# Performance work log

Hardware: AMD Instinct MI355X
Metric: run time of the kernel (lower is better)

Reference implementation:

```python
import jax, jax.numpy as jnp
import numpy as np

WINDOW_SIZE = 11
SIGMA = 1.5
C1 = 0.01 ** 2
C2 = 0.03 ** 2


def _gaussian_window(window_size: int = WINDOW_SIZE, sigma: float = SIGMA) -> jnp.ndarray:
    x = np.arange(window_size)
    g = np.exp(-((x - window_size // 2) ** 2) / (2.0 * sigma ** 2)).astype(np.float32)
    g = g / g.sum()
    w2d = np.outer(g, g)  # [K, K]
    return jnp.asarray(w2d[None, None])  # [1, 1, K, K] (OIHW)


def _blur(x: jnp.ndarray, window: jnp.ndarray) -> jnp.ndarray:
    pad = WINDOW_SIZE // 2
    return jax.lax.conv_general_dilated(
        x, window, window_strides=(1, 1),
        padding=[(pad, pad), (pad, pad)],
        dimension_numbers=("NCHW", "OIHW", "NCHW"))


def setup_inputs() -> dict:
    key = jax.random.key(0)
    k1, k2 = jax.random.split(key)
    shape = (16, 1, 1024, 1024)
    img1 = jax.random.uniform(k1, shape, dtype=jnp.float32)
    img2 = jax.random.uniform(k2, shape, dtype=jnp.float32)
    return {"img1": img1, "img2": img2}


def reference(img1, img2) -> jnp.ndarray:
    window = _gaussian_window().astype(img1.dtype)
    mu1 = _blur(img1, window)
    mu2 = _blur(img2, window)
    mu1_sq = mu1 * mu1
    mu2_sq = mu2 * mu2
    mu1_mu2 = mu1 * mu2
    sigma1_sq = _blur(img1 * img1, window) - mu1_sq
    sigma2_sq = _blur(img2 * img2, window) - mu2_sq
    sigma12 = _blur(img1 * img2, window) - mu1_mu2
    ssim_map = ((2 * mu1_mu2 + C1) * (2 * sigma12 + C2)) / (
        (mu1_sq + mu2_sq + C1) * (sigma1_sq + sigma2_sq + C2))
    return 1.0 - ssim_map.mean()
```

## Files before the change

### kernel.cpp

```cpp
#include <hip/hip_runtime.h>
#include <hip/hip_fp16.h>

#define IMG_H 1024
#define IMG_W 1024
#define NIMG  16
#define RAD   5
#define KW    11
#define TX    64
#define STRIP 128
#define ASTEP 16
#define BSTEP 32
#define HBROWS (STRIP + 2*RAD)
#define RING  48
#define PADW  68
#define NPIX  (NIMG * IMG_H * IMG_W)

__device__ __forceinline__ float gw(int k) {
    constexpr float G[KW] = {
        0.00102838f, 0.00759876f, 0.03600077f, 0.10936070f, 0.21300554f,
        0.26601173f,
        0.21300554f, 0.10936070f, 0.03600077f, 0.00759876f, 0.00102838f};
    return G[k];
}

__device__ __forceinline__ unsigned h2u(__half2 v) {
    union { __half2 h; unsigned u; } c; c.h = v; return c.u;
}
__device__ __forceinline__ __half2 u2h(unsigned v) {
    union { unsigned u; __half2 h; } c; c.u = v; return c.h;
}
__device__ __forceinline__ __half2 hsel(const unsigned* hw, int idx) {
    unsigned r;
    if (idx & 1) r = (hw[idx >> 1] >> 16) | (hw[(idx >> 1) + 1] << 16);
    else         r = hw[idx >> 1];
    return u2h(r);
}

__global__ __launch_bounds__(256, 8) void ssim_strip_kernel(
        const float* __restrict__ img1, const float* __restrict__ img2,
        float* __restrict__ partial, int atomic_mode) {
    __shared__ __align__(16) __half hb[5][RING][PADW];
    __shared__ float wsum[4];

    const int t = threadIdx.x;
    const int tile_x = blockIdx.x * TX;
    const int tile_y = blockIdx.y * STRIP;
    const size_t img_off = (size_t)blockIdx.z * (IMG_H * IMG_W);
    const float* p1 = img1 + img_off;
    const float* p2 = img2 + img_off;

    const bool x_ok = (tile_x >= 8) && (tile_x + 72 <= IMG_W);

    auto phaseA = [&](int a) {
        const int tr = t >> 4;
        const int g4 = t & 15;
        const int h = ASTEP * a + tr;
        if (h >= HBROWS) return;
        int rr = h;
        if (rr >= 96) rr -= 96;
        else if (rr >= RING) rr -= RING;
        const int gr = tile_y + h - RAD;
        const int gc0 = tile_x + g4 * 4 - 8;
        const bool row_ok = (tile_y + ASTEP * a - RAD >= 0) &&
                            (tile_y + ASTEP * a + ASTEP - 1 - RAD < IMG_H);
        unsigned hwx[10], hwy[10];
        if (x_ok && row_ok) {
            const size_t base = (size_t)gr * IMG_W + gc0;
#pragma unroll
            for (int w = 0; w < 5; ++w) {
                const float4 xa = *reinterpret_cast<const float4*>(p1 + base + 4 * w);
                const float4 ya = *reinterpret_cast<const float4*>(p2 + base + 4 * w);
                hwx[2 * w]     = h2u(__floats2half2_rn(xa.x, xa.y));
                hwx[2 * w + 1] = h2u(__floats2half2_rn(xa.z, xa.w));
                hwy[2 * w]     = h2u(__floats2half2_rn(ya.x, ya.y));
                hwy[2 * w + 1] = h2u(__floats2half2_rn(ya.z, ya.w));
            }
        } else {
            const bool rowok = ((unsigned)gr < (unsigned)IMG_H);
            const float* row1 = p1 + (size_t)gr * IMG_W;
            const float* row2 = p2 + (size_t)gr * IMG_W;
#pragma unroll
            for (int w = 0; w < 5; ++w) {
                const int gc = gc0 + 4 * w;
                float4 xa = make_float4(0.f, 0.f, 0.f, 0.f);
                float4 ya = make_float4(0.f, 0.f, 0.f, 0.f);
                if (rowok) {
                    if (gc >= 0 && gc <= IMG_W - 4) {
                        xa = *reinterpret_cast<const float4*>(row1 + gc);
                        ya = *reinterpret_cast<const float4*>(row2 + gc);
                    } else if (gc > -4 && gc < IMG_W) {
                        float* ex = &xa.x;
                        float* ey = &ya.x;
#pragma unroll
                        for (int j = 0; j < 4; ++j) {
                            int g = gc + j;
                            if ((unsigned)g < (unsigned)IMG_W) {
                                ex[j] = row1[g];
                                ey[j] = row2[g];
                            }
                        }
                    }
                }
                hwx[2 * w]     = h2u(__floats2half2_rn(xa.x, xa.y));
                hwx[2 * w + 1] = h2u(__floats2half2_rn(xa.z, xa.w));
                hwy[2 * w]     = h2u(__floats2half2_rn(ya.x, ya.y));
                hwy[2 * w + 1] = h2u(__floats2half2_rn(ya.z, ya.w));
            }
        }
        __half2 A0[2], A1[2], A2[2], A3[2], A4[2];
#pragma unroll
        for (int p = 0; p < 2; ++p)
            A0[p] = A1[p] = A2[p] = A3[p] = A4[p] = u2h(0u);
#pragma unroll
        for (int k = 0; k < KW; ++k) {
            const __half2 g2 = __float2half2_rn(gw(k));
#pragma unroll
            for (int p = 0; p < 2; ++p) {
                const int idx = 2 * p + 3 + k;
                const __half2 X = hsel(hwx, idx);
                const __half2 Y = hsel(hwy, idx);
                A0[p] = __hfma2(g2, X, A0[p]);
                A1[p] = __hfma2(g2, Y, A1[p]);
                const __half2 gx = __hmul2(g2, X);
                const __half2 gy = __hmul2(g2, Y);
                A2[p] = __hfma2(gx, X, A2[p]);
                A3[p] = __hfma2(gy, Y, A3[p]);
                A4[p] = __hfma2(gx, Y, A4[p]);
            }
        }
        *reinterpret_cast<uint2*>(&hb[0][rr][g4 * 4]) = make_uint2(h2u(A0[0]), h2u(A0[1]));
        *reinterpret_cast<uint2*>(&hb[1][rr][g4 * 4]) = make_uint2(h2u(A1[0]), h2u(A1[1]));
        *reinterpret_cast<uint2*>(&hb[2][rr][g4 * 4]) = make_uint2(h2u(A2[0]), h2u(A2[1]));
        *reinterpret_cast<uint2*>(&hb[3][rr][g4 * 4]) = make_uint2(h2u(A3[0]), h2u(A3[1]));
        *reinterpret_cast<uint2*>(&hb[4][rr][g4 * 4]) = make_uint2(h2u(A4[0]), h2u(A4[1]));
    };

    float lsum = 0.f;

    auto phaseB = [&](int s) {
        __half2 gh2[KW];
#pragma unroll
        for (int k = 0; k < KW; ++k) gh2[k] = __float2half2_rn(gw(k));

        const int rbase = (BSTEP * s) % RING;
        const int slot = t & 15;
        const int r2 = (t >> 4) * 2;
        __half2 acc[5][2][2];
#pragma unroll
        for (int q = 0; q < 5; ++q)
#pragma unroll
            for (int rl = 0; rl < 2; ++rl)
#pragma unroll
                for (int cp = 0; cp < 2; ++cp)
                    acc[q][rl][cp] = u2h(0u);

#pragma unroll
        for (int q = 0; q < 5; ++q) {
#pragma unroll
            for (int k = 0; k < KW + 1; ++k) {
                int r = rbase + r2 + k;
                if (r >= RING) r -= RING;
                const uint2 rv =
                    *reinterpret_cast<const uint2*>(&hb[q][r][slot * 4]);
                __half2 h0 = u2h(rv.x);
                __half2 h1 = u2h(rv.y);
                if (k < KW) {
                    acc[q][0][0] = __hfma2(gh2[k], h0, acc[q][0][0]);
                    acc[q][0][1] = __hfma2(gh2[k], h1, acc[q][0][1]);
                }
                if (k > 0) {
                    acc[q][1][0] = __hfma2(gh2[k - 1], h0, acc[q][1][0]);
                    acc[q][1][1] = __hfma2(gh2[k - 1], h1, acc[q][1][1]);
                }
            }
        }

        const float C1 = 0.0001f;
        const float C2 = 0.0009f;
#pragma unroll
        for (int rl = 0; rl < 2; ++rl) {
#pragma unroll
            for (int cp = 0; cp < 2; ++cp) {
                float2 m1p  = __half22float2(acc[0][rl][cp]);
                float2 m2p  = __half22float2(acc[1][rl][cp]);
                float2 b11p = __half22float2(acc[2][rl][cp]);
                float2 b22p = __half22float2(acc[3][rl][cp]);
                float2 b12p = __half22float2(acc[4][rl][cp]);
#pragma unroll
                for (int e = 0; e < 2; ++e) {
                    float m1 = e ? m1p.y : m1p.x;
                    float m2 = e ? m2p.y : m2p.x;
                    float b11 = e ? b11p.y : b11p.x;
                    float b22 = e ? b22p.y : b22p.x;
                    float b12 = e ? b12p.y : b12p.x;
                    float m1s = m1 * m1;
                    float m2s = m2 * m2;
                    float m12 = m1 * m2;
                    float num = (2.f * m12 + C1) * (2.f * (b12 - m12) + C2);
                    float den = (m1s + m2s + C1) *
                                ((b11 - m1s) + (b22 - m2s) + C2);
                    lsum = fmaf(num, __builtin_amdgcn_rcpf(den), lsum);
                }
            }
        }
    };

#pragma unroll 1
    for (int a = 0; a < 9; ++a) {
        phaseA(a);
        __syncthreads();
        if (a >= 2 && ((a & 1) == 0)) {
            phaseB((a - 2) >> 1);
            __syncthreads();
        }
    }

#pragma unroll
    for (int off = 32; off > 0; off >>= 1)
        lsum += __shfl_down(lsum, off, 64);
    if ((t & 63) == 0) wsum[t >> 6] = lsum;
    __syncthreads();
    if (t == 0) {
        float s = wsum[0] + wsum[1] + wsum[2] + wsum[3];
        if (atomic_mode) {
            atomicAdd(partial, s);
        } else {
            int bid = (blockIdx.z * gridDim.y + blockIdx.y) * gridDim.x + blockIdx.x;
            partial[bid] = s;
        }
    }
}

__global__ __launch_bounds__(256) void ssim_reduce_kernel(
        const float* __restrict__ partial, int n, float* __restrict__ out) {
    float s = 0.f;
    for (int i = threadIdx.x; i < n; i += 256) s += partial[i];
#pragma unroll
    for (int off = 32; off > 0; off >>= 1)
        s += __shfl_down(s, off, 64);
    __shared__ float ws[4];
    if ((threadIdx.x & 63) == 0) ws[threadIdx.x >> 6] = s;
    __syncthreads();
    if (threadIdx.x == 0) {
        float tot = ws[0] + ws[1] + ws[2] + ws[3];
        out[0] = 1.f - tot / (float)NPIX;
    }
}

extern "C" void kernel_launch(void* const* d_in, const int* in_sizes, int n_in,
                              void* d_out, int out_size, void* d_ws, size_t ws_size,
                              hipStream_t stream) {
    const float* img1 = (const float*)d_in[0];
    const float* img2 = (const float*)d_in[1];
    float* out = (float*)d_out;
    float* partial = (float*)d_ws;

    dim3 grid(IMG_W / TX, IMG_H / STRIP, NIMG);
    const int nblocks = (IMG_W / TX) * (IMG_H / STRIP) * NIMG;
    const size_t needed = (size_t)nblocks * sizeof(float);

    if (ws_size >= needed) {
        ssim_strip_kernel<<<grid, 256, 0, stream>>>(img1, img2, partial, 0);
        ssim_reduce_kernel<<<1, 256, 0, stream>>>(partial, nblocks, out);
    } else {
        hipMemsetAsync(d_ws, 0, sizeof(float), stream);
        ssim_strip_kernel<<<grid, 256, 0, stream>>>(img1, img2, partial, 1);
        ssim_reduce_kernel<<<1, 256, 0, stream>>>(partial, 1, out);
    }
}
```

Baseline: 79.56 us.

## Prefetch next strip rows into registers while computing the vertical SSIM pass

Splits the horizontal pass into a global-load step and a convert/blur/store step, so raw float4 row data can be loaded into registers before the vertical-blur and SSIM phase runs and consumed after the barrier. The aim is to hide global memory latency behind the phase-B compute instead of stalling at the start of each horizontal step. The loop is unrolled into a software pipeline with fewer barriers. Launch bounds drop from 8 to 4 blocks per CU to leave room for the extra live registers, which risks lower occupancy.

New measurement: 165.5 us. 108% more time.

```diff
diff --git a/kernel.cpp b/kernel.cpp
--- a/kernel.cpp
+++ b/kernel.cpp
@@ -36,7 +36,12 @@
     return u2h(r);
 }
 
-__global__ __launch_bounds__(256, 8) void ssim_strip_kernel(
+struct Raw {
+    float4 x0, x1, x2, x3, x4;
+    float4 y0, y1, y2, y3, y4;
+};
+
+__global__ __launch_bounds__(256, 4) void ssim_strip_kernel(
         const float* __restrict__ img1, const float* __restrict__ img2,
         float* __restrict__ partial, int atomic_mode) {
     __shared__ __align__(16) __half hb[5][RING][PADW];
@@ -51,7 +56,65 @@
 
     const bool x_ok = (tile_x >= 8) && (tile_x + 72 <= IMG_W);
 
-    auto phaseA = [&](int a) {
+    auto ldpair = [&](const float* r1, const float* r2, int gc, bool rowok,
+                      float4& xa, float4& ya) {
+        xa = make_float4(0.f, 0.f, 0.f, 0.f);
+        ya = make_float4(0.f, 0.f, 0.f, 0.f);
+        if (rowok) {
+            if (gc >= 0 && gc <= IMG_W - 4) {
+                xa = *reinterpret_cast<const float4*>(r1 + gc);
+                ya = *reinterpret_cast<const float4*>(r2 + gc);
+            } else if (gc > -4 && gc < IMG_W) {
+                float* ex = &xa.x;
+                float* ey = &ya.x;
+#pragma unroll
+                for (int j = 0; j < 4; ++j) {
+                    int g = gc + j;
+                    if ((unsigned)g < (unsigned)IMG_W) {
+                        ex[j] = r1[g];
+                        ey[j] = r2[g];
+                    }
+                }
+            }
+        }
+    };
+
+    auto loadRaw = [&](int a) -> Raw {
+        Raw rw;
+        const int tr = t >> 4;
+        const int g4 = t & 15;
+        const int h = ASTEP * a + tr;
+        const int gr = tile_y + h - RAD;
+        const int gc0 = tile_x + g4 * 4 - 8;
+        const bool row_ok = (tile_y + ASTEP * a - RAD >= 0) &&
+                            (tile_y + ASTEP * a + ASTEP - 1 - RAD < IMG_H);
+        if (h < HBROWS && x_ok && row_ok) {
+            const float* b1 = p1 + (size_t)gr * IMG_W + gc0;
+            const float* b2 = p2 + (size_t)gr * IMG_W + gc0;
+            rw.x0 = *reinterpret_cast<const float4*>(b1);
+            rw.x1 = *reinterpret_cast<const float4*>(b1 + 4);
+            rw.x2 = *reinterpret_cast<const float4*>(b1 + 8);
+            rw.x3 = *reinterpret_cast<const float4*>(b1 + 12);
+            rw.x4 = *reinterpret_cast<const float4*>(b1 + 16);
+            rw.y0 = *reinterpret_cast<const float4*>(b2);
+            rw.y1 = *reinterpret_cast<const float4*>(b2 + 4);
+            rw.y2 = *reinterpret_cast<const float4*>(b2 + 8);
+            rw.y3 = *reinterpret_cast<const float4*>(b2 + 12);
+            rw.y4 = *reinterpret_cast<const float4*>(b2 + 16);
+        } else {
+            const bool rowok = (h < HBROWS) && ((unsigned)gr < (unsigned)IMG_H);
+            const float* r1 = p1 + (size_t)gr * IMG_W;
+            const float* r2 = p2 + (size_t)gr * IMG_W;
+            ldpair(r1, r2, gc0,      rowok, rw.x0, rw.y0);
+            ldpair(r1, r2, gc0 + 4,  rowok, rw.x1, rw.y1);
+            ldpair(r1, r2, gc0 + 8,  rowok, rw.x2, rw.y2);
+            ldpair(r1, r2, gc0 + 12, rowok, rw.x3, rw.y3);
+            ldpair(r1, r2, gc0 + 16, rowok, rw.x4, rw.y4);
+        }
+        return rw;
+    };
+
+    auto blurStore = [&](const Raw& rw, int a) {
         const int tr = t >> 4;
         const int g4 = t & 15;
         const int h = ASTEP * a + tr;
@@ -59,54 +122,28 @@
         int rr = h;
         if (rr >= 96) rr -= 96;
         else if (rr >= RING) rr -= RING;
-        const int gr = tile_y + h - RAD;
-        const int gc0 = tile_x + g4 * 4 - 8;
-        const bool row_ok = (tile_y + ASTEP * a - RAD >= 0) &&
-                            (tile_y + ASTEP * a + ASTEP - 1 - RAD < IMG_H);
         unsigned hwx[10], hwy[10];
-        if (x_ok && row_ok) {
-            const size_t base = (size_t)gr * IMG_W + gc0;
-#pragma unroll
-            for (int w = 0; w < 5; ++w) {
-                const float4 xa = *reinterpret_cast<const float4*>(p1 + base + 4 * w);
-                const float4 ya = *reinterpret_cast<const float4*>(p2 + base + 4 * w);
-                hwx[2 * w]     = h2u(__floats2half2_rn(xa.x, xa.y));
-                hwx[2 * w + 1] = h2u(__floats2half2_rn(xa.z, xa.w));
-                hwy[2 * w]     = h2u(__floats2half2_rn(ya.x, ya.y));
-                hwy[2 * w + 1] = h2u(__floats2half2_rn(ya.z, ya.w));
-            }
-        } else {
-            const bool rowok = ((unsigned)gr < (unsigned)IMG_H);
-            const float* row1 = p1 + (size_t)gr * IMG_W;
-            const float* row2 = p2 + (size_t)gr * IMG_W;
-#pragma unroll
-            for (int w = 0; w < 5; ++w) {
-                const int gc = gc0 + 4 * w;
-                float4 xa = make_float4(0.f, 0.f, 0.f, 0.f);
-                float4 ya = make_float4(0.f, 0.f, 0.f, 0.f);
-                if (rowok) {
-                    if (gc >= 0 && gc <= IMG_W - 4) {
-                        xa = *reinterpret_cast<const float4*>(row1 + gc);
-                        ya = *reinterpret_cast<const float4*>(row2 + gc);
-                    } else if (gc > -4 && gc < IMG_W) {
-                        float* ex = &xa.x;
-                        float* ey = &ya.x;
-#pragma unroll
-                        for (int j = 0; j < 4; ++j) {
-                            int g = gc + j;
-                            if ((unsigned)g < (unsigned)IMG_W) {
-                                ex[j] = row1[g];
-                                ey[j] = row2[g];
-                            }
-                        }
-                    }
-                }
-                hwx[2 * w]     = h2u(__floats2half2_rn(xa.x, xa.y));
-                hwx[2 * w + 1] = h2u(__floats2half2_rn(xa.z, xa.w));
-                hwy[2 * w]     = h2u(__floats2half2_rn(ya.x, ya.y));
-                hwy[2 * w + 1] = h2u(__floats2half2_rn(ya.z, ya.w));
-            }
-        }
+        hwx[0] = h2u(__floats2half2_rn(rw.x0.x, rw.x0.y));
+        hwx[1] = h2u(__floats2half2_rn(rw.x0.z, rw.x0.w));
+        hwx[2] = h2u(__floats2half2_rn(rw.x1.x, rw.x1.y));
+        hwx[3] = h2u(__floats2half2_rn(rw.x1.z, rw.x1.w));
+        hwx[4] = h2u(__floats2half2_rn(rw.x2.x, rw.x2.y));
+        hwx[5] = h2u(__floats2half2_rn(rw.x2.z, rw.x2.w));
+        hwx[6] = h2u(__floats2half2_rn(rw.x3.x, rw.x3.y));
+        hwx[7] = h2u(__floats2half2_rn(rw.x3.z, rw.x3.w));
+        hwx[8] = h2u(__floats2half2_rn(rw.x4.x, rw.x4.y));
+        hwx[9] = h2u(__floats2half2_rn(rw.x4.z, rw.x4.w));
+        hwy[0] = h2u(__floats2half2_rn(rw.y0.x, rw.y0.y));
+        hwy[1] = h2u(__floats2half2_rn(rw.y0.z, rw.y0.w));
+        hwy[2] = h2u(__floats2half2_rn(rw.y1.x, rw.y1.y));
+        hwy[3] = h2u(__floats2half2_rn(rw.y1.z, rw.y1.w));
+        hwy[4] = h2u(__floats2half2_rn(rw.y2.x, rw.y2.y));
+        hwy[5] = h2u(__floats2half2_rn(rw.y2.z, rw.y2.w));
+        hwy[6] = h2u(__floats2half2_rn(rw.y3.x, rw.y3.y));
+        hwy[7] = h2u(__floats2half2_rn(rw.y3.z, rw.y3.w));
+        hwy[8] = h2u(__floats2half2_rn(rw.y4.x, rw.y4.y));
+        hwy[9] = h2u(__floats2half2_rn(rw.y4.z, rw.y4.w));
+
         __half2 A0[2], A1[2], A2[2], A3[2], A4[2];
 #pragma unroll
         for (int p = 0; p < 2; ++p)
@@ -205,15 +242,27 @@
         }
     };
 
+    {
+        Raw ra = loadRaw(0);
+        Raw rb = loadRaw(1);
+        blurStore(ra, 0);
+        ra = loadRaw(2);
+        blurStore(rb, 1);
+        blurStore(ra, 2);
+    }
+    __syncthreads();
+
 #pragma unroll 1
-    for (int a = 0; a < 9; ++a) {
-        phaseA(a);
+    for (int s = 0; s < 3; ++s) {
+        Raw ra = loadRaw(3 + 2 * s);
+        phaseB(s);
         __syncthreads();
-        if (a >= 2 && ((a & 1) == 0)) {
-            phaseB((a - 2) >> 1);
-            __syncthreads();
-        }
-    }
+        blurStore(ra, 3 + 2 * s);
+        Raw rb = loadRaw(4 + 2 * s);
+        blurStore(rb, 4 + 2 * s);
+        __syncthreads();
+    }
+    phaseB(3);
 
 #pragma unroll
     for (int off = 32; off > 0; off >>= 1)
```
